# Kernel tuning notes

Hardware: AMD Instinct MI355X
Metric: run time of the kernel (lower is better)

The kernel has to match this reference:

```python
import jax, jax.numpy as jnp
import numpy as np

N_NODES = 100000
N_EDGES = 3200000
N_GRAPHS = 64
EPS = 1e-5


def setup_inputs() -> dict:
    key = jax.random.key(0)
    ks = jax.random.split(key, 14)
    x = jax.random.normal(ks[0], (N_NODES, 3), dtype=jnp.float32)
    edge_index = jax.random.randint(ks[1], (2, N_EDGES), 0, N_NODES, dtype=jnp.int32)
    edge_attr = jax.random.uniform(ks[2], (N_EDGES, 2), dtype=jnp.float32)
    batch = jnp.sort(jax.random.randint(ks[3], (N_NODES,), 0, N_GRAPHS, dtype=jnp.int32))
    # SplineConv weights: [K=4 kernels, C_in, C_out]
    W1 = jax.random.normal(ks[4], (4, 3, 8), dtype=jnp.float32) * 0.4
    W2 = jax.random.normal(ks[5], (4, 8, 16), dtype=jnp.float32) * 0.25
    W3 = jax.random.normal(ks[6], (4, 16, 32), dtype=jnp.float32) * 0.2
    g1 = jnp.ones((8,), jnp.float32); b1 = jnp.zeros((8,), jnp.float32)
    g2 = jnp.ones((16,), jnp.float32); b2 = jnp.zeros((16,), jnp.float32)
    g3 = jnp.ones((32,), jnp.float32); b3 = jnp.zeros((32,), jnp.float32)
    fc_w = jax.random.normal(ks[7], (10, 32), dtype=jnp.float32) * 0.15  # Linear(32,10,bias=False)
    return dict(x=x, edge_index=edge_index, edge_attr=edge_attr, batch=batch,
                W1=W1, W2=W2, W3=W3, g1=g1, b1=b1, g2=g2, b2=b2, g3=g3, b3=b3,
                fc_w=fc_w)


def _basis(edge_attr):
    # degree-1 open B-spline, kernel_size=2 per dim, dim=2 -> 4 fixed kernel indices
    u = jnp.clip(edge_attr, 0.0, 1.0)
    u0, u1 = u[:, 0], u[:, 1]
    return jnp.stack([(1 - u0) * (1 - u1),  # kernel (0,0)
                      u0 * (1 - u1),        # kernel (1,0)
                      (1 - u0) * u1,        # kernel (0,1)
                      u0 * u1], axis=-1)    # kernel (1,1)  -> [E,4]


def _spline_conv(x, src, dst, basis, W, inv_deg):
    # gather source feats, basis-weighted kernel mix, scatter-mean to targets
    msg = jnp.einsum('ek,ec,kcd->ed', basis, x[src], W)  # [E, C_out]
    agg = jax.ops.segment_sum(msg, dst, num_segments=x.shape[0])
    return agg * inv_deg


def _bn(x, g, b):
    mu = jnp.mean(x, axis=0)
    var = jnp.mean((x - mu) ** 2, axis=0)  # biased, training-mode BatchNorm
    return (x - mu) * jax.lax.rsqrt(var + EPS) * g + b


def reference(x, edge_index, edge_attr, batch, W1, W2, W3, g1, b1, g2, b2, g3, b3, fc_w):
    src, dst = edge_index[0], edge_index[1]
    B = _basis(edge_attr)
    n = x.shape[0]
    deg = jax.ops.segment_sum(jnp.ones((src.shape[0],), x.dtype), dst, num_segments=n)
    inv_deg = (1.0 / jnp.maximum(deg, 1.0))[:, None]

    h = _bn(jax.nn.elu(_spline_conv(x, src, dst, B, W1, inv_deg)), g1, b1)
    h = _bn(jax.nn.elu(_spline_conv(h, src, dst, B, W2, inv_deg)), g2, b2)
    h = _bn(jax.nn.elu(_spline_conv(h, src, dst, B, W3, inv_deg)), g3, b3)

    pooled = jax.ops.segment_sum(h, batch, num_segments=N_GRAPHS)
    cnt = jax.ops.segment_sum(jnp.ones((n,), h.dtype), batch, num_segments=N_GRAPHS)
    pooled = pooled / jnp.maximum(cnt, 1.0)[:, None]  # global_mean_pool -> [G, 32]
    return pooled @ fc_w.T  # [G, 10]
```

## Files before the change

### kernel.cpp

```cpp
#include <hip/hip_runtime.h>
#include <hip/hip_fp16.h>

#define N_NODES 100000
#define N_EDGES 3200000
#define N_GRAPHS 64
constexpr int NC    = 196;
constexpr int PBLK  = 256;
constexpr int CHUNK = N_EDGES / PBLK;
constexpr int NBLK  = (N_NODES + 255) / 256;
constexpr int LBLK  = N_NODES / 32;
constexpr int FCAP  = 18432;
#define EPS 1e-5f

constexpr size_t OFF_CNTG   = 0x0;
constexpr size_t OFF_BNS1   = 0x400;
constexpr size_t OFF_BNS2   = 0x500;
constexpr size_t OFF_BNS3   = 0x700;
constexpr size_t OFF_POOLED = 0x1000;
constexpr size_t ZERO_BYTES = 0x3000;
constexpr size_t OFF_CBASE  = 0x4000;
constexpr size_t OFF_BTOT   = 0x5000;
constexpr size_t OFF_ROWPTR = 0x10000;
constexpr size_t OFF_HISTM  = 0x80000;
constexpr size_t OFF_ES     = 0x200000;
constexpr size_t OFF_EP     = 0x1B00000;
constexpr size_t OFF_T1     = 0x3400000;
constexpr size_t OFF_T2     = 0x3800000;
constexpr size_t OFF_T3     = 0x4000000;

__global__ void cnt_kernel(const int* __restrict__ batch, int* __restrict__ cntg) {
    int g = threadIdx.x;
    if (g >= N_GRAPHS) return;
    int lo0 = 0, hi0 = N_NODES;
    while (lo0 < hi0) { int m = (lo0 + hi0) >> 1; if (batch[m] < g) lo0 = m + 1; else hi0 = m; }
    int lo1 = lo0, hi1 = N_NODES;
    while (lo1 < hi1) { int m = (lo1 + hi1) >> 1; if (batch[m] < g + 1) lo1 = m + 1; else hi1 = m; }
    cntg[g] = lo1 - lo0;
}

__global__ __launch_bounds__(256) void k_hist(const int* __restrict__ dst,
                                              int* __restrict__ histM) {
    __shared__ int h[NC];
    for (int i = threadIdx.x; i < NC; i += 256) h[i] = 0;
    __syncthreads();
    int base = blockIdx.x * CHUNK;
    for (int i = threadIdx.x; i < CHUNK; i += 256)
        atomicAdd(&h[dst[base + i] >> 9], 1);
    __syncthreads();
    for (int i = threadIdx.x; i < NC; i += 256)
        histM[i * PBLK + blockIdx.x] = h[i];
}

__global__ __launch_bounds__(256) void k_scan1(int* __restrict__ histM,
                                               int* __restrict__ btot) {
    __shared__ int sd[256];
    int b = blockIdx.x, t = threadIdx.x;
    int v = histM[b * PBLK + t];
    sd[t] = v;
    __syncthreads();
    for (int off = 1; off < 256; off <<= 1) {
        int x = (t >= off) ? sd[t - off] : 0;
        __syncthreads();
        sd[t] += x;
        __syncthreads();
    }
    histM[b * PBLK + t] = sd[t] - v;
    if (t == 255) btot[b] = sd[255];
}

__global__ __launch_bounds__(256) void k_scan2(const int* __restrict__ btot,
                                               int* __restrict__ cbase) {
    __shared__ int sd[256];
    int t = threadIdx.x;
    int v = (t < NC) ? btot[t] : 0;
    sd[t] = v;
    __syncthreads();
    for (int off = 1; off < 256; off <<= 1) {
        int x = (t >= off) ? sd[t - off] : 0;
        __syncthreads();
        sd[t] += x;
        __syncthreads();
    }
    if (t < NC) cbase[t] = sd[t] - v;
    if (t == 0) cbase[NC] = N_EDGES;
}

__global__ __launch_bounds__(256) void k_part(const int* __restrict__ src,
                                              const int* __restrict__ dst,
                                              const float2* __restrict__ ea,
                                              const int* __restrict__ histM,
                                              const int* __restrict__ cbase,
                                              uint2* __restrict__ Es) {
    __shared__ int cur[NC];
    for (int i = threadIdx.x; i < NC; i += 256)
        cur[i] = cbase[i] + histM[i * PBLK + blockIdx.x];
    __syncthreads();
    int base = blockIdx.x * CHUNK;
    for (int i = threadIdx.x; i < CHUNK; i += 256) {
        int e = base + i;
        int d = dst[e];
        float2 u = ea[e];
        float u0 = fminf(fmaxf(u.x, 0.f), 1.f);
        float u1 = fminf(fmaxf(u.y, 0.f), 1.f);
        unsigned u0q = __float2uint_rn(u0 * 524287.f);
        unsigned u1q = __float2uint_rn(u1 * 524287.f);
        unsigned w0 = (unsigned)src[e] | ((u0q & 0x7FFFu) << 17);
        unsigned w1 = (u0q >> 15) | (u1q << 4) | ((unsigned)(d & 511) << 23);
        int pos = atomicAdd(&cur[d >> 9], 1);
        Es[pos] = make_uint2(w0, w1);
    }
}

__global__ __launch_bounds__(1024) void k_fine(const uint2* __restrict__ Es,
                                               const int* __restrict__ cbase,
                                               int* __restrict__ rowptr,
                                               uint2* __restrict__ Ep) {
    extern __shared__ uint2 rec[];
    __shared__ int cnt[512];
    __shared__ int cur[512];
    __shared__ int sd[512];
    int b = blockIdx.x, t = threadIdx.x;
    int lo = cbase[b], hi = cbase[b + 1];
    int m = hi - lo;
    if (t < 512) cnt[t] = 0;
    __syncthreads();
    for (int i = lo + t; i < hi; i += 1024)
        atomicAdd(&cnt[Es[i].y >> 23], 1);
    __syncthreads();
    if (t < 512) sd[t] = cnt[t];
    __syncthreads();
    for (int off = 1; off < 512; off <<= 1) {
        int x = (t < 512 && t >= off) ? sd[t - off] : 0;
        __syncthreads();
        if (t < 512) sd[t] += x;
        __syncthreads();
    }
    if (t < 512) {
        int excl = sd[t] - cnt[t];
        cur[t] = excl;
        int n = b * 512 + t;
        if (n < N_NODES) rowptr[n] = lo + excl;
    }
    if (b == NC - 1 && t == 0) rowptr[N_NODES] = N_EDGES;
    __syncthreads();
    if (m <= FCAP) {
        for (int i = lo + t; i < hi; i += 1024) {
            uint2 r = Es[i];
            int pos = atomicAdd(&cur[r.y >> 23], 1);
            rec[pos] = r;
        }
        __syncthreads();
        for (int i = t; i < m; i += 1024)
            Ep[lo + i] = rec[i];
    } else {
        for (int i = lo + t; i < hi; i += 1024) {
            uint2 r = Es[i];
            int pos = atomicAdd(&cur[r.y >> 23], 1);
            Ep[lo + pos] = r;
        }
    }
}

#define DECODE_EDGE(r)                                              \
    int s = r.x & 0x1FFFF;                                          \
    unsigned u0q = (r.x >> 17) | ((r.y & 0xFu) << 15);              \
    unsigned u1q = (r.y >> 4) & 0x7FFFFu;                           \
    float u0 = u0q * (1.f / 524287.f);                              \
    float u1 = u1q * (1.f / 524287.f);                              \
    float nu0 = 1.f - u0, nu1 = 1.f - u1;                           \
    float b0 = nu0 * nu1, b1 = u0 * nu1, b2 = nu0 * u1, b3 = u0 * u1;

__global__ __launch_bounds__(256) void layer1_kernel(const float* __restrict__ xin,
                                                     const int* __restrict__ rowptr,
                                                     const uint2* __restrict__ Ep,
                                                     const float* __restrict__ W,
                                                     __half* __restrict__ tout) {
    __shared__ float Wl[96];
    for (int i = threadIdx.x; i < 96; i += 256) Wl[i] = W[i];
    __syncthreads();
    int lane8 = threadIdx.x & 7;
    int n = blockIdx.x * 32 + (threadIdx.x >> 3);
    int e0 = rowptr[n], e1 = rowptr[n + 1];
    float z[12];
#pragma unroll
    for (int i = 0; i < 12; ++i) z[i] = 0.f;
#pragma unroll 2
    for (int j = e0 + lane8; j < e1; j += 8) {
        uint2 r = Ep[j];
        DECODE_EDGE(r)
        float x0 = xin[s * 3 + 0], x1 = xin[s * 3 + 1], x2 = xin[s * 3 + 2];
        z[0] += b0 * x0; z[1]  += b0 * x1; z[2]  += b0 * x2;
        z[3] += b1 * x0; z[4]  += b1 * x1; z[5]  += b1 * x2;
        z[6] += b2 * x0; z[7]  += b2 * x1; z[8]  += b2 * x2;
        z[9] += b3 * x0; z[10] += b3 * x1; z[11] += b3 * x2;
    }
#pragma unroll
    for (int i = 0; i < 12; ++i) {
        z[i] += __shfl_xor(z[i], 4);
        z[i] += __shfl_xor(z[i], 2);
        z[i] += __shfl_xor(z[i], 1);
    }
    float y = 0.f;
#pragma unroll
    for (int kc = 0; kc < 12; ++kc) y += z[kc] * Wl[kc * 8 + lane8];
    float invd = 1.f / fmaxf((float)(e1 - e0), 1.f);
    float v = y * invd;
    v = v > 0.f ? v : expm1f(v);
    tout[(size_t)n * 8 + lane8] = __float2half_rn(v);
}

__global__ __launch_bounds__(256) void layer2_kernel(const __half* __restrict__ xin,
                                                     const float* __restrict__ bns,
                                                     const float* __restrict__ g,
                                                     const float* __restrict__ bb,
                                                     const int* __restrict__ rowptr,
                                                     const uint2* __restrict__ Ep,
                                                     const float* __restrict__ W,
                                                     __half* __restrict__ tout) {
    __shared__ float scA[8], shA[8];
    __shared__ float4 Wl[140];
    __shared__ float shW[64];
    int t = threadIdx.x;
    if (t < 8) {
        float mu = bns[t] * (1.f / N_NODES);
        float var = fmaxf(bns[8 + t] * (1.f / N_NODES) - mu * mu, 0.f);
        float s = g[t] * rsqrtf(var + EPS);
        scA[t] = s;
        shA[t] = bb[t] - mu * s;
    }
    __syncthreads();
    if (t < 128) {
        int k = t >> 5, d4 = (t >> 3) & 3, c = t & 7;
        float4 w = ((const float4*)W)[(k * 8 + c) * 4 + d4];
        float s = scA[c];
        Wl[k * 35 + d4 * 9 + c] = make_float4(w.x * s, w.y * s, w.z * s, w.w * s);
    } else if (t < 192) {
        int j = t - 128;
        int k = j >> 4, d = j & 15;
        float acc = 0.f;
#pragma unroll
        for (int c = 0; c < 8; ++c) acc += shA[c] * W[(k * 8 + c) * 16 + d];
        shW[j] = acc;
    }
    __syncthreads();

    int lane8 = t & 7;
    int kq = lane8 & 3, h = lane8 >> 2;
    int ch = kq & 1;
    int eo = lane8 >> 1;
    int n = blockIdx.x * 32 + (t >> 3);
    int e0 = rowptr[n], e1 = rowptr[n + 1];
    float z[16], S[4];
#pragma unroll
    for (int i = 0; i < 16; ++i) z[i] = 0.f;
#pragma unroll
    for (int i = 0; i < 4; ++i) S[i] = 0.f;
#pragma unroll 2
    for (int j = e0 + eo; j < e1; j += 4) {
        uint2 r = Ep[j];
        DECODE_EDGE(r)
        uint2 hv = *(const uint2*)(xin + (size_t)s * 8 + 4 * ch);
        float2 f0 = __half22float2(*(__half2*)&hv.x);
        float2 f1 = __half22float2(*(__half2*)&hv.y);
        S[0] += b0; S[1] += b1; S[2] += b2; S[3] += b3;
        z[0]  += b0 * f0.x; z[1]  += b0 * f0.y; z[2]  += b0 * f1.x; z[3]  += b0 * f1.y;
        z[4]  += b1 * f0.x; z[5]  += b1 * f0.y; z[6]  += b1 * f1.x; z[7]  += b1 * f1.y;
        z[8]  += b2 * f0.x; z[9]  += b2 * f0.y; z[10] += b2 * f1.x; z[11] += b2 * f1.y;
        z[12] += b3 * f0.x; z[13] += b3 * f0.y; z[14] += b3 * f1.x; z[15] += b3 * f1.y;
    }
#pragma unroll
    for (int i = 0; i < 16; ++i) { z[i] += __shfl_xor(z[i], 4); z[i] += __shfl_xor(z[i], 2); }
#pragma unroll
    for (int i = 0; i < 4; ++i)  { S[i] += __shfl_xor(S[i], 4); S[i] += __shfl_xor(S[i], 2); }

    int laneW = 18 * h + 4 * ch;
    float y[8];
#pragma unroll
    for (int i = 0; i < 8; ++i) y[i] = 0.f;
#pragma unroll
    for (int k = 0; k < 4; ++k)
#pragma unroll
        for (int i = 0; i < 4; ++i) {
            float zc = z[k * 4 + i];
            int base = k * 35 + i + laneW;
#pragma unroll
            for (int d4 = 0; d4 < 2; ++d4) {
                float4 w = Wl[base + 9 * d4];
                y[4 * d4 + 0] += zc * w.x; y[4 * d4 + 1] += zc * w.y;
                y[4 * d4 + 2] += zc * w.z; y[4 * d4 + 3] += zc * w.w;
            }
        }
    float y1[4];
#pragma unroll
    for (int i = 0; i < 4; ++i) {
        float a = y[i]     + __shfl_xor(y[i],     1);
        float b = y[4 + i] + __shfl_xor(y[4 + i], 1);
        y1[i] = ch ? b : a;
    }
    int qb = (kq >> 1) & 1;
    float f0 = qb ? y1[2] : y1[0];
    float f1 = qb ? y1[3] : y1[1];
    int d = h * 8 + ch * 4 + qb * 2;
    f0 += S[0] * shW[d]     + S[1] * shW[16 + d]     + S[2] * shW[32 + d]     + S[3] * shW[48 + d];
    f1 += S[0] * shW[d + 1] + S[1] * shW[16 + d + 1] + S[2] * shW[32 + d + 1] + S[3] * shW[48 + d + 1];
    float invd = 1.f / fmaxf((float)(e1 - e0), 1.f);
    f0 *= invd; f1 *= invd;
    f0 = f0 > 0.f ? f0 : expm1f(f0);
    f1 = f1 > 0.f ? f1 : expm1f(f1);
    *(__half2*)(tout + (size_t)n * 16 + d) = __floats2half2_rn(f0, f1);
}

__global__ __launch_bounds__(256) void layer3_kernel(const __half* __restrict__ xin,
                                                     const float* __restrict__ bns,
                                                     const float* __restrict__ g,
                                                     const float* __restrict__ bb,
                                                     const int* __restrict__ rowptr,
                                                     const uint2* __restrict__ Ep,
                                                     const float* __restrict__ W,
                                                     __half* __restrict__ tout) {
    __shared__ float scA[16], shA[16];
    __shared__ float4 Wl[580];
    __shared__ float shW[128];
    int t = threadIdx.x;
    if (t < 16) {
        float mu = bns[t] * (1.f / N_NODES);
        float var = fmaxf(bns[16 + t] * (1.f / N_NODES) - mu * mu, 0.f);
        float s = g[t] * rsqrtf(var + EPS);
        scA[t] = s;
        shA[t] = bb[t] - mu * s;
    }
    __syncthreads();
    for (int i = t; i < 512; i += 256) {
        int k = i >> 7, d4 = (i >> 4) & 7, c = i & 15;
        float4 w = ((const float4*)W)[(k * 16 + c) * 8 + d4];
        float s = scA[c];
        Wl[k * 145 + d4 * 18 + (d4 >> 2) + c + 2 * (c >> 3)] =
            make_float4(w.x * s, w.y * s, w.z * s, w.w * s);
    }
    if (t < 128) {
        int k = t >> 5, d = t & 31;
        float acc = 0.f;
#pragma unroll
        for (int c = 0; c < 16; ++c) acc += shA[c] * W[(k * 16 + c) * 32 + d];
        shW[t] = acc;
    }
    __syncthreads();

    int lane8 = t & 7;
    int kq = lane8 & 3, h = lane8 >> 2;
    int n = blockIdx.x * 32 + (t >> 3);
    int e0 = rowptr[n], e1 = rowptr[n + 1];
    float z[16], S[4];
#pragma unroll
    for (int i = 0; i < 16; ++i) z[i] = 0.f;
#pragma unroll
    for (int i = 0; i < 4; ++i) S[i] = 0.f;
#pragma unroll 2
    for (int j = e0 + h; j < e1; j += 2) {
        uint2 r = Ep[j];
        DECODE_EDGE(r)
        uint2 hv = *(const uint2*)(xin + (size_t)s * 16 + 4 * kq);
        float2 f0 = __half22float2(*(__half2*)&hv.x);
        float2 f1 = __half22float2(*(__half2*)&hv.y);
        S[0] += b0; S[1] += b1; S[2] += b2; S[3] += b3;
        z[0]  += b0 * f0.x; z[1]  += b0 * f0.y; z[2]  += b0 * f1.x; z[3]  += b0 * f1.y;
        z[4]  += b1 * f0.x; z[5]  += b1 * f0.y; z[6]  += b1 * f1.x; z[7]  += b1 * f1.y;
        z[8]  += b2 * f0.x; z[9]  += b2 * f0.y; z[10] += b2 * f1.x; z[11] += b2 * f1.y;
        z[12] += b3 * f0.x; z[13] += b3 * f0.y; z[14] += b3 * f1.x; z[15] += b3 * f1.y;
    }
#pragma unroll
    for (int i = 0; i < 16; ++i) z[i] += __shfl_xor(z[i], 4);
#pragma unroll
    for (int i = 0; i < 4; ++i)  S[i] += __shfl_xor(S[i], 4);

    int laneW = 4 * kq + 2 * (kq >> 1) + 73 * h;
    float y[16];
#pragma unroll
    for (int i = 0; i < 16; ++i) y[i] = 0.f;
#pragma unroll
    for (int k = 0; k < 4; ++k)
#pragma unroll
        for (int i = 0; i < 4; ++i) {
            float zc = z[k * 4 + i];
            int base = k * 145 + i + laneW;
#pragma unroll
            for (int d4 = 0; d4 < 4; ++d4) {
                float4 w = Wl[base + 18 * d4];
                y[4 * d4 + 0] += zc * w.x; y[4 * d4 + 1] += zc * w.y;
                y[4 * d4 + 2] += zc * w.z; y[4 * d4 + 3] += zc * w.w;
            }
        }
    float y1[8];
#pragma unroll
    for (int i = 0; i < 8; ++i) {
        float a = y[i]     + __shfl_xor(y[i],     1);
        float b = y[8 + i] + __shfl_xor(y[8 + i], 1);
        y1[i] = (kq & 1) ? b : a;
    }
    float y2[4];
#pragma unroll
    for (int i = 0; i < 4; ++i) {
        float a = y1[i]     + __shfl_xor(y1[i],     2);
        float b = y1[4 + i] + __shfl_xor(y1[4 + i], 2);
        y2[i] = (kq & 2) ? b : a;
    }
    int d = h * 16 + (kq & 1) * 8 + ((kq >> 1) & 1) * 4;
#pragma unroll
    for (int i = 0; i < 4; ++i)
        y2[i] += S[0] * shW[d + i] + S[1] * shW[32 + d + i] +
                 S[2] * shW[64 + d + i] + S[3] * shW[96 + d + i];
    float invd = 1.f / fmaxf((float)(e1 - e0), 1.f);
#pragma unroll
    for (int i = 0; i < 4; ++i) {
        float v = y2[i] * invd;
        y2[i] = v > 0.f ? v : expm1f(v);
    }
    __half2 h01 = __floats2half2_rn(y2[0], y2[1]);
    __half2 h23 = __floats2half2_rn(y2[2], y2[3]);
    uint2 st;
    st.x = *(unsigned*)&h01;
    st.y = *(unsigned*)&h23;
    *(uint2*)(tout + (size_t)n * 32 + d) = st;
}

template <int COUT>
__global__ __launch_bounds__(256) void bnstats_kernel(const __half* __restrict__ t,
                                                      float* __restrict__ sums) {
    constexpr int ROWS = 256 / COUT;
    int ch = threadIdx.x % COUT;
    int r = threadIdx.x / COUT;
    float s = 0.f, q = 0.f;
    for (int n = blockIdx.x * ROWS + r; n < N_NODES; n += gridDim.x * ROWS) {
        float v = __half2float(t[(size_t)n * COUT + ch]);
        s += v;
        q += v * v;
    }
    __shared__ float ls[256], lq[256];
    ls[threadIdx.x] = s; lq[threadIdx.x] = q;
    __syncthreads();
    for (int off = 128; off >= COUT; off >>= 1) {
        if (threadIdx.x < off) {
            ls[threadIdx.x] += ls[threadIdx.x + off];
            lq[threadIdx.x] += lq[threadIdx.x + off];
        }
        __syncthreads();
    }
    if (threadIdx.x < COUT) {
        atomicAdd(&sums[ch], ls[threadIdx.x]);
        atomicAdd(&sums[COUT + ch], lq[threadIdx.x]);
    }
}

__global__ __launch_bounds__(256) void pool_kernel(const __half* __restrict__ t3,
                                                   const int* __restrict__ batch,
                                                   float* __restrict__ pooled) {
    __shared__ float tile[256][33];
    __shared__ int lb[256];
    int n = blockIdx.x * 256 + threadIdx.x;
    int valid = N_NODES - blockIdx.x * 256;
    if (valid > 256) valid = 256;
    if (n < N_NODES) {
        const uint4* r = (const uint4*)(t3 + (size_t)n * 32);
#pragma unroll
        for (int i = 0; i < 4; ++i) {
            uint4 v = r[i];
            float2 a = __half22float2(*(__half2*)&v.x);
            float2 b = __half22float2(*(__half2*)&v.y);
            float2 c = __half22float2(*(__half2*)&v.z);
            float2 d = __half22float2(*(__half2*)&v.w);
            tile[threadIdx.x][8 * i + 0] = a.x;
            tile[threadIdx.x][8 * i + 1] = a.y;
            tile[threadIdx.x][8 * i + 2] = b.x;
            tile[threadIdx.x][8 * i + 3] = b.y;
            tile[threadIdx.x][8 * i + 4] = c.x;
            tile[threadIdx.x][8 * i + 5] = c.y;
            tile[threadIdx.x][8 * i + 6] = d.x;
            tile[threadIdx.x][8 * i + 7] = d.y;
        }
        lb[threadIdx.x] = batch[n];
    }
    __syncthreads();
    if (threadIdx.x < 32) {
        int ch = threadIdx.x;
        float run = 0.f;
        int gp = lb[0];
        for (int r = 0; r < valid; ++r) {
            int g = lb[r];
            if (g != gp) {
                atomicAdd(&pooled[gp * 32 + ch], run);
                run = 0.f;
                gp = g;
            }
            run += tile[r][ch];
        }
        atomicAdd(&pooled[gp * 32 + ch], run);
    }
}

__global__ void final_kernel(const float* __restrict__ pooled, const int* __restrict__ cntg,
                             const float* __restrict__ bns, const float* __restrict__ g,
                             const float* __restrict__ bb, const float* __restrict__ fcw,
                             float* __restrict__ out) {
    __shared__ float sc3[32], sh3[32];
    if (threadIdx.x < 32) {
        int c = threadIdx.x;
        float mu = bns[c] * (1.f / N_NODES);
        float var = fmaxf(bns[32 + c] * (1.f / N_NODES) - mu * mu, 0.f);
        float s = g[c] * rsqrtf(var + EPS);
        sc3[c] = s;
        sh3[c] = bb[c] - mu * s;
    }
    __syncthreads();
    int i = threadIdx.x;
    if (i >= N_GRAPHS * 10) return;
    int gi = i / 10, o = i % 10;
    float rc = 1.f / fmaxf((float)cntg[gi], 1.f);
    float acc = 0.f;
#pragma unroll
    for (int d = 0; d < 32; ++d) {
        float pm = sc3[d] * (pooled[gi * 32 + d] * rc) + sh3[d];
        acc += pm * fcw[o * 32 + d];
    }
    out[i] = acc;
}

extern "C" void kernel_launch(void* const* d_in, const int* in_sizes, int n_in,
                              void* d_out, int out_size, void* d_ws, size_t ws_size,
                              hipStream_t stream) {
    const float* x   = (const float*)d_in[0];
    const int*   ei  = (const int*)d_in[1];
    const float* ea  = (const float*)d_in[2];
    const int*   bat = (const int*)d_in[3];
    const float* W1  = (const float*)d_in[4];
    const float* W2  = (const float*)d_in[5];
    const float* W3  = (const float*)d_in[6];
    const float* g1  = (const float*)d_in[7];
    const float* b1  = (const float*)d_in[8];
    const float* g2  = (const float*)d_in[9];
    const float* b2  = (const float*)d_in[10];
    const float* g3  = (const float*)d_in[11];
    const float* b3  = (const float*)d_in[12];
    const float* fcw = (const float*)d_in[13];
    float* out = (float*)d_out;
    char* ws = (char*)d_ws;

    int*    cntg   = (int*)(ws + OFF_CNTG);
    float*  bns1   = (float*)(ws + OFF_BNS1);
    float*  bns2   = (float*)(ws + OFF_BNS2);
    float*  bns3   = (float*)(ws + OFF_BNS3);
    float*  pooled = (float*)(ws + OFF_POOLED);
    int*    cbase  = (int*)(ws + OFF_CBASE);
    int*    btot   = (int*)(ws + OFF_BTOT);
    int*    rowptr = (int*)(ws + OFF_ROWPTR);
    int*    histM  = (int*)(ws + OFF_HISTM);
    uint2*  Es     = (uint2*)(ws + OFF_ES);
    uint2*  Ep     = (uint2*)(ws + OFF_EP);
    __half* t1     = (__half*)(ws + OFF_T1);
    __half* t2     = (__half*)(ws + OFF_T2);
    __half* t3     = (__half*)(ws + OFF_T3);

    const int* src = ei;
    const int* dst = ei + N_EDGES;

    hipFuncSetAttribute((const void*)k_fine,
                        hipFuncAttributeMaxDynamicSharedMemorySize, FCAP * 8);

    hipMemsetAsync(ws, 0, ZERO_BYTES, stream);

    cnt_kernel<<<1, 64, 0, stream>>>(bat, cntg);
    k_hist<<<PBLK, 256, 0, stream>>>(dst, histM);
    k_scan1<<<NC, 256, 0, stream>>>(histM, btot);
    k_scan2<<<1, 256, 0, stream>>>(btot, cbase);
    k_part<<<PBLK, 256, 0, stream>>>(src, dst, (const float2*)ea, histM, cbase, Es);
    k_fine<<<NC, 1024, FCAP * 8, stream>>>(Es, cbase, rowptr, Ep);

    layer1_kernel<<<LBLK, 256, 0, stream>>>(x, rowptr, Ep, W1, t1);
    bnstats_kernel<8><<<256, 256, 0, stream>>>(t1, bns1);

    layer2_kernel<<<LBLK, 256, 0, stream>>>(t1, bns1, g1, b1, rowptr, Ep, W2, t2);
    bnstats_kernel<16><<<256, 256, 0, stream>>>(t2, bns2);

    layer3_kernel<<<LBLK, 256, 0, stream>>>(t2, bns2, g2, b2, rowptr, Ep, W3, t3);
    bnstats_kernel<32><<<256, 256, 0, stream>>>(t3, bns3);

    pool_kernel<<<NBLK, 256, 0, stream>>>(t3, bat, pooled);
    final_kernel<<<1, 640, 0, stream>>>(pooled, cntg, bns3, g3, b3, fcw, out);
}
```

Measured before the change: 224.1 us.

## Pad layer-1 input to fp16x4, use packed float2 FMAs, fold graph counts into final kernel

Adds a pre-pass that converts the 3-channel fp32 node features into padded 4-wide fp16 rows, so layer 1 gathers one 8-byte aligned load per edge instead of three scalar float loads. Layers 2 and 3 rewrite their edge accumulation and weight-mixing loops with 2-wide float vectors, aiming for packed FMA instructions. The per-graph count binary search moves out of its own kernel into the final kernel. The fp16 input adds rounding error to layer 1, and the packed math relies on the compiler emitting packed FMAs.

```diff
diff --git a/kernel.cpp b/kernel.cpp
--- a/kernel.cpp
+++ b/kernel.cpp
@@ -12,7 +12,10 @@
 constexpr int FCAP  = 18432;
 #define EPS 1e-5f
 
-constexpr size_t OFF_CNTG   = 0x0;
+typedef float f2 __attribute__((ext_vector_type(2)));
+static __device__ __forceinline__ f2 mkf2(float a, float b) { f2 r; r.x = a; r.y = b; return r; }
+static __device__ __forceinline__ unsigned h2u(__half2 v) { unsigned r; __builtin_memcpy(&r, &v, 4); return r; }
+
 constexpr size_t OFF_BNS1   = 0x400;
 constexpr size_t OFF_BNS2   = 0x500;
 constexpr size_t OFF_BNS3   = 0x700;
@@ -22,20 +25,20 @@
 constexpr size_t OFF_BTOT   = 0x5000;
 constexpr size_t OFF_ROWPTR = 0x10000;
 constexpr size_t OFF_HISTM  = 0x80000;
+constexpr size_t OFF_XP     = 0x100000;
 constexpr size_t OFF_ES     = 0x200000;
 constexpr size_t OFF_EP     = 0x1B00000;
 constexpr size_t OFF_T1     = 0x3400000;
 constexpr size_t OFF_T2     = 0x3800000;
 constexpr size_t OFF_T3     = 0x4000000;
 
-__global__ void cnt_kernel(const int* __restrict__ batch, int* __restrict__ cntg) {
-    int g = threadIdx.x;
-    if (g >= N_GRAPHS) return;
-    int lo0 = 0, hi0 = N_NODES;
-    while (lo0 < hi0) { int m = (lo0 + hi0) >> 1; if (batch[m] < g) lo0 = m + 1; else hi0 = m; }
-    int lo1 = lo0, hi1 = N_NODES;
-    while (lo1 < hi1) { int m = (lo1 + hi1) >> 1; if (batch[m] < g + 1) lo1 = m + 1; else hi1 = m; }
-    cntg[g] = lo1 - lo0;
+__global__ __launch_bounds__(256) void xpad_kernel(const float* __restrict__ x,
+                                                   __half* __restrict__ xp) {
+    int n = blockIdx.x * 256 + threadIdx.x;
+    if (n >= N_NODES) return;
+    __half2 a = __floats2half2_rn(x[n * 3 + 0], x[n * 3 + 1]);
+    __half2 b = __floats2half2_rn(x[n * 3 + 2], 0.f);
+    *(uint2*)(xp + (size_t)n * 4) = make_uint2(h2u(a), h2u(b));
 }
 
 __global__ __launch_bounds__(256) void k_hist(const int* __restrict__ dst,
@@ -170,7 +173,7 @@
     float nu0 = 1.f - u0, nu1 = 1.f - u1;                           \
     float b0 = nu0 * nu1, b1 = u0 * nu1, b2 = nu0 * u1, b3 = u0 * u1;
 
-__global__ __launch_bounds__(256) void layer1_kernel(const float* __restrict__ xin,
+__global__ __launch_bounds__(256) void layer1_kernel(const __half* __restrict__ xp,
                                                      const int* __restrict__ rowptr,
                                                      const uint2* __restrict__ Ep,
                                                      const float* __restrict__ W,
@@ -188,7 +191,10 @@
     for (int j = e0 + lane8; j < e1; j += 8) {
         uint2 r = Ep[j];
         DECODE_EDGE(r)
-        float x0 = xin[s * 3 + 0], x1 = xin[s * 3 + 1], x2 = xin[s * 3 + 2];
+        uint2 hv = *(const uint2*)(xp + (size_t)s * 4);
+        float2 p0 = __half22float2(*(__half2*)&hv.x);
+        float2 p1 = __half22float2(*(__half2*)&hv.y);
+        float x0 = p0.x, x1 = p0.y, x2 = p1.x;
         z[0] += b0 * x0; z[1]  += b0 * x1; z[2]  += b0 * x2;
         z[3] += b1 * x0; z[4]  += b1 * x1; z[5]  += b1 * x2;
         z[6] += b2 * x0; z[7]  += b2 * x1; z[8]  += b2 * x2;
@@ -250,9 +256,10 @@
     int eo = lane8 >> 1;
     int n = blockIdx.x * 32 + (t >> 3);
     int e0 = rowptr[n], e1 = rowptr[n + 1];
-    float z[16], S[4];
-#pragma unroll
-    for (int i = 0; i < 16; ++i) z[i] = 0.f;
+    f2 zf[8];
+    float S[4];
+#pragma unroll
+    for (int i = 0; i < 8; ++i) zf[i] = mkf2(0.f, 0.f);
 #pragma unroll
     for (int i = 0; i < 4; ++i) S[i] = 0.f;
 #pragma unroll 2
@@ -260,36 +267,49 @@
         uint2 r = Ep[j];
         DECODE_EDGE(r)
         uint2 hv = *(const uint2*)(xin + (size_t)s * 8 + 4 * ch);
-        float2 f0 = __half22float2(*(__half2*)&hv.x);
-        float2 f1 = __half22float2(*(__half2*)&hv.y);
+        float2 p0 = __half22float2(*(__half2*)&hv.x);
+        float2 p1 = __half22float2(*(__half2*)&hv.y);
+        f2 x01 = mkf2(p0.x, p0.y), x23 = mkf2(p1.x, p1.y);
         S[0] += b0; S[1] += b1; S[2] += b2; S[3] += b3;
-        z[0]  += b0 * f0.x; z[1]  += b0 * f0.y; z[2]  += b0 * f1.x; z[3]  += b0 * f1.y;
-        z[4]  += b1 * f0.x; z[5]  += b1 * f0.y; z[6]  += b1 * f1.x; z[7]  += b1 * f1.y;
-        z[8]  += b2 * f0.x; z[9]  += b2 * f0.y; z[10] += b2 * f1.x; z[11] += b2 * f1.y;
-        z[12] += b3 * f0.x; z[13] += b3 * f0.y; z[14] += b3 * f1.x; z[15] += b3 * f1.y;
-    }
-#pragma unroll
-    for (int i = 0; i < 16; ++i) { z[i] += __shfl_xor(z[i], 4); z[i] += __shfl_xor(z[i], 2); }
-#pragma unroll
-    for (int i = 0; i < 4; ++i)  { S[i] += __shfl_xor(S[i], 4); S[i] += __shfl_xor(S[i], 2); }
+        f2 bbv;
+        bbv = mkf2(b0, b0); zf[0] += bbv * x01; zf[1] += bbv * x23;
+        bbv = mkf2(b1, b1); zf[2] += bbv * x01; zf[3] += bbv * x23;
+        bbv = mkf2(b2, b2); zf[4] += bbv * x01; zf[5] += bbv * x23;
+        bbv = mkf2(b3, b3); zf[6] += bbv * x01; zf[7] += bbv * x23;
+    }
+#pragma unroll
+    for (int i = 0; i < 8; ++i) {
+        zf[i].x += __shfl_xor(zf[i].x, 4); zf[i].y += __shfl_xor(zf[i].y, 4);
+        zf[i].x += __shfl_xor(zf[i].x, 2); zf[i].y += __shfl_xor(zf[i].y, 2);
+    }
+#pragma unroll
+    for (int i = 0; i < 4; ++i) { S[i] += __shfl_xor(S[i], 4); S[i] += __shfl_xor(S[i], 2); }
 
     int laneW = 18 * h + 4 * ch;
-    float y[8];
-#pragma unroll
-    for (int i = 0; i < 8; ++i) y[i] = 0.f;
-#pragma unroll
-    for (int k = 0; k < 4; ++k)
+    f2 ya[2], yb[2];
+#pragma unroll
+    for (int i = 0; i < 2; ++i) { ya[i] = mkf2(0.f, 0.f); yb[i] = mkf2(0.f, 0.f); }
+#pragma unroll
+    for (int k = 0; k < 4; ++k) {
+        float zs[4] = {zf[2 * k].x, zf[2 * k].y, zf[2 * k + 1].x, zf[2 * k + 1].y};
 #pragma unroll
         for (int i = 0; i < 4; ++i) {
-            float zc = z[k * 4 + i];
+            f2 zsp = mkf2(zs[i], zs[i]);
             int base = k * 35 + i + laneW;
 #pragma unroll
             for (int d4 = 0; d4 < 2; ++d4) {
                 float4 w = Wl[base + 9 * d4];
-                y[4 * d4 + 0] += zc * w.x; y[4 * d4 + 1] += zc * w.y;
-                y[4 * d4 + 2] += zc * w.z; y[4 * d4 + 3] += zc * w.w;
+                ya[d4] += zsp * mkf2(w.x, w.y);
+                yb[d4] += zsp * mkf2(w.z, w.w);
             }
         }
+    }
+    float y[8];
+#pragma unroll
+    for (int d4 = 0; d4 < 2; ++d4) {
+        y[4 * d4 + 0] = ya[d4].x; y[4 * d4 + 1] = ya[d4].y;
+        y[4 * d4 + 2] = yb[d4].x; y[4 * d4 + 3] = yb[d4].y;
+    }
     float y1[4];
 #pragma unroll
     for (int i = 0; i < 4; ++i) {
@@ -350,9 +370,10 @@
     int kq = lane8 & 3, h = lane8 >> 2;
     int n = blockIdx.x * 32 + (t >> 3);
     int e0 = rowptr[n], e1 = rowptr[n + 1];
-    float z[16], S[4];
-#pragma unroll
-    for (int i = 0; i < 16; ++i) z[i] = 0.f;
+    f2 zf[8];
+    float S[4];
+#pragma unroll
+    for (int i = 0; i < 8; ++i) zf[i] = mkf2(0.f, 0.f);
 #pragma unroll
     for (int i = 0; i < 4; ++i) S[i] = 0.f;
 #pragma unroll 2
@@ -360,36 +381,49 @@
         uint2 r = Ep[j];
         DECODE_EDGE(r)
         uint2 hv = *(const uint2*)(xin + (size_t)s * 16 + 4 * kq);
-        float2 f0 = __half22float2(*(__half2*)&hv.x);
-        float2 f1 = __half22float2(*(__half2*)&hv.y);
+        float2 p0 = __half22float2(*(__half2*)&hv.x);
+        float2 p1 = __half22float2(*(__half2*)&hv.y);
+        f2 x01 = mkf2(p0.x, p0.y), x23 = mkf2(p1.x, p1.y);
         S[0] += b0; S[1] += b1; S[2] += b2; S[3] += b3;
-        z[0]  += b0 * f0.x; z[1]  += b0 * f0.y; z[2]  += b0 * f1.x; z[3]  += b0 * f1.y;
-        z[4]  += b1 * f0.x; z[5]  += b1 * f0.y; z[6]  += b1 * f1.x; z[7]  += b1 * f1.y;
-        z[8]  += b2 * f0.x; z[9]  += b2 * f0.y; z[10] += b2 * f1.x; z[11] += b2 * f1.y;
-        z[12] += b3 * f0.x; z[13] += b3 * f0.y; z[14] += b3 * f1.x; z[15] += b3 * f1.y;
-    }
-#pragma unroll
-    for (int i = 0; i < 16; ++i) z[i] += __shfl_xor(z[i], 4);
-#pragma unroll
-    for (int i = 0; i < 4; ++i)  S[i] += __shfl_xor(S[i], 4);
+        f2 bbv;
+        bbv = mkf2(b0, b0); zf[0] += bbv * x01; zf[1] += bbv * x23;
+        bbv = mkf2(b1, b1); zf[2] += bbv * x01; zf[3] += bbv * x23;
+        bbv = mkf2(b2, b2); zf[4] += bbv * x01; zf[5] += bbv * x23;
+        bbv = mkf2(b3, b3); zf[6] += bbv * x01; zf[7] += bbv * x23;
+    }
+#pragma unroll
+    for (int i = 0; i < 8; ++i) {
+        zf[i].x += __shfl_xor(zf[i].x, 4);
+        zf[i].y += __shfl_xor(zf[i].y, 4);
+    }
+#pragma unroll
+    for (int i = 0; i < 4; ++i) S[i] += __shfl_xor(S[i], 4);
 
     int laneW = 4 * kq + 2 * (kq >> 1) + 73 * h;
-    float y[16];
-#pragma unroll
-    for (int i = 0; i < 16; ++i) y[i] = 0.f;
-#pragma unroll
-    for (int k = 0; k < 4; ++k)
+    f2 ya[4], yb[4];
+#pragma unroll
+    for (int i = 0; i < 4; ++i) { ya[i] = mkf2(0.f, 0.f); yb[i] = mkf2(0.f, 0.f); }
+#pragma unroll
+    for (int k = 0; k < 4; ++k) {
+        float zs[4] = {zf[2 * k].x, zf[2 * k].y, zf[2 * k + 1].x, zf[2 * k + 1].y};
 #pragma unroll
         for (int i = 0; i < 4; ++i) {
-            float zc = z[k * 4 + i];
+            f2 zsp = mkf2(zs[i], zs[i]);
             int base = k * 145 + i + laneW;
 #pragma unroll
             for (int d4 = 0; d4 < 4; ++d4) {
                 float4 w = Wl[base + 18 * d4];
-                y[4 * d4 + 0] += zc * w.x; y[4 * d4 + 1] += zc * w.y;
-                y[4 * d4 + 2] += zc * w.z; y[4 * d4 + 3] += zc * w.w;
+                ya[d4] += zsp * mkf2(w.x, w.y);
+                yb[d4] += zsp * mkf2(w.z, w.w);
             }
         }
+    }
+    float y[16];
+#pragma unroll
+    for (int d4 = 0; d4 < 4; ++d4) {
+        y[4 * d4 + 0] = ya[d4].x; y[4 * d4 + 1] = ya[d4].y;
+        y[4 * d4 + 2] = yb[d4].x; y[4 * d4 + 3] = yb[d4].y;
+    }
     float y1[8];
 #pragma unroll
     for (int i = 0; i < 8; ++i) {
@@ -418,8 +452,8 @@
     __half2 h01 = __floats2half2_rn(y2[0], y2[1]);
     __half2 h23 = __floats2half2_rn(y2[2], y2[3]);
     uint2 st;
-    st.x = *(unsigned*)&h01;
-    st.y = *(unsigned*)&h23;
+    st.x = h2u(h01);
+    st.y = h2u(h23);
     *(uint2*)(tout + (size_t)n * 32 + d) = st;
 }
 
@@ -497,24 +531,32 @@
     }
 }
 
-__global__ void final_kernel(const float* __restrict__ pooled, const int* __restrict__ cntg,
+__global__ void final_kernel(const float* __restrict__ pooled, const int* __restrict__ batch,
                              const float* __restrict__ bns, const float* __restrict__ g,
                              const float* __restrict__ bb, const float* __restrict__ fcw,
                              float* __restrict__ out) {
     __shared__ float sc3[32], sh3[32];
-    if (threadIdx.x < 32) {
-        int c = threadIdx.x;
-        float mu = bns[c] * (1.f / N_NODES);
-        float var = fmaxf(bns[32 + c] * (1.f / N_NODES) - mu * mu, 0.f);
-        float s = g[c] * rsqrtf(var + EPS);
-        sc3[c] = s;
-        sh3[c] = bb[c] - mu * s;
-    }
-    __syncthreads();
-    int i = threadIdx.x;
+    __shared__ float rcg[64];
+    int t = threadIdx.x;
+    if (t < 32) {
+        float mu = bns[t] * (1.f / N_NODES);
+        float var = fmaxf(bns[32 + t] * (1.f / N_NODES) - mu * mu, 0.f);
+        float s = g[t] * rsqrtf(var + EPS);
+        sc3[t] = s;
+        sh3[t] = bb[t] - mu * s;
+    } else if (t >= 64 && t < 128) {
+        int gr = t - 64;
+        int lo0 = 0, hi0 = N_NODES;
+        while (lo0 < hi0) { int m = (lo0 + hi0) >> 1; if (batch[m] < gr) lo0 = m + 1; else hi0 = m; }
+        int lo1 = lo0, hi1 = N_NODES;
+        while (lo1 < hi1) { int m = (lo1 + hi1) >> 1; if (batch[m] < gr + 1) lo1 = m + 1; else hi1 = m; }
+        rcg[gr] = 1.f / fmaxf((float)(lo1 - lo0), 1.f);
+    }
+    __syncthreads();
+    int i = t;
     if (i >= N_GRAPHS * 10) return;
     int gi = i / 10, o = i % 10;
-    float rc = 1.f / fmaxf((float)cntg[gi], 1.f);
+    float rc = rcg[gi];
     float acc = 0.f;
 #pragma unroll
     for (int d = 0; d < 32; ++d) {
@@ -544,7 +586,6 @@
     float* out = (float*)d_out;
     char* ws = (char*)d_ws;
 
-    int*    cntg   = (int*)(ws + OFF_CNTG);
     float*  bns1   = (float*)(ws + OFF_BNS1);
     float*  bns2   = (float*)(ws + OFF_BNS2);
     float*  bns3   = (float*)(ws + OFF_BNS3);
@@ -555,6 +596,7 @@
     int*    histM  = (int*)(ws + OFF_HISTM);
     uint2*  Es     = (uint2*)(ws + OFF_ES);
     uint2*  Ep     = (uint2*)(ws + OFF_EP);
+    __half* xp     = (__half*)(ws + OFF_XP);
     __half* t1     = (__half*)(ws + OFF_T1);
     __half* t2     = (__half*)(ws + OFF_T2);
     __half* t3     = (__half*)(ws + OFF_T3);
@@ -567,14 +609,14 @@
 
     hipMemsetAsync(ws, 0, ZERO_BYTES, stream);
 
-    cnt_kernel<<<1, 64, 0, stream>>>(bat, cntg);
+    xpad_kernel<<<NBLK, 256, 0, stream>>>(x, xp);
     k_hist<<<PBLK, 256, 0, stream>>>(dst, histM);
     k_scan1<<<NC, 256, 0, stream>>>(histM, btot);
     k_scan2<<<1, 256, 0, stream>>>(btot, cbase);
     k_part<<<PBLK, 256, 0, stream>>>(src, dst, (const float2*)ea, histM, cbase, Es);
     k_fine<<<NC, 1024, FCAP * 8, stream>>>(Es, cbase, rowptr, Ep);
 
-    layer1_kernel<<<LBLK, 256, 0, stream>>>(x, rowptr, Ep, W1, t1);
+    layer1_kernel<<<LBLK, 256, 0, stream>>>(xp, rowptr, Ep, W1, t1);
     bnstats_kernel<8><<<256, 256, 0, stream>>>(t1, bns1);
 
     layer2_kernel<<<LBLK, 256, 0, stream>>>(t1, bns1, g1, b1, rowptr, Ep, W2, t2);
@@ -584,5 +626,5 @@
     bnstats_kernel<32><<<256, 256, 0, stream>>>(t3, bns3);
 
     pool_kernel<<<NBLK, 256, 0, stream>>>(t3, bat, pooled);
-    final_kernel<<<1, 640, 0, stream>>>(pooled, cntg, bns3, g3, b3, fcw, out);
-}
+    final_kernel<<<1, 640, 0, stream>>>(pooled, bat, bns3, g3, b3, fcw, out);
+}
```

Result: no change. 224.3 us (+0.1%).
